# Kernel tuning notes

Measured on AMD Instinct MI355X. Metric: run time of the kernel, lower is better.

The kernel has to match this reference:

```python
import jax, jax.numpy as jnp
import numpy as np

N_NODES = 100000
D_FEAT = 64
HIDDEN = 64
N_CLASSES = 16
N_EDGES = 1600000


def setup_inputs() -> dict:
    key = jax.random.key(0)
    ks = jax.random.split(key, 8)
    x = jax.random.normal(ks[0], (N_NODES, D_FEAT), dtype=jnp.float32)
    edge_index = jax.random.randint(ks[1], (2, N_EDGES), 0, N_NODES, dtype=jnp.int64)
    s1 = 1.0 / np.sqrt(D_FEAT)
    s2 = 1.0 / np.sqrt(HIDDEN)
    W1 = jax.random.uniform(ks[2], (D_FEAT, HIDDEN), jnp.float32, -s1, s1)
    b1 = jnp.zeros((HIDDEN,), jnp.float32)
    W2 = jax.random.uniform(ks[3], (HIDDEN, HIDDEN), jnp.float32, -s2, s2)
    b2 = jnp.zeros((HIDDEN,), jnp.float32)
    Wfc = jax.random.uniform(ks[4], (HIDDEN, N_CLASSES), jnp.float32, -s2, s2)
    bfc = jax.random.uniform(ks[5], (N_CLASSES,), jnp.float32, -s2, s2)
    return {"x": x, "edge_index": edge_index, "W1": W1, "b1": b1,
            "W2": W2, "b2": b2, "Wfc": Wfc, "bfc": bfc}


def reference(x, edge_index, W1, b1, W2, b2, Wfc, bfc):
    N = x.shape[0]
    loops = jnp.arange(N, dtype=edge_index.dtype)
    # GCNConv adds self-loops by default
    src = jnp.concatenate([edge_index[0], loops])  # message source j
    dst = jnp.concatenate([edge_index[1], loops])  # aggregation target i
    # symmetric normalization: D^{-1/2} (A + I) D^{-1/2}, degree counted on targets
    deg = jax.ops.segment_sum(jnp.ones_like(dst, dtype=x.dtype), dst, num_segments=N)
    dinv = jnp.where(deg > 0, jax.lax.rsqrt(deg), 0.0)
    norm = dinv[src] * dinv[dst]  # [E+N]

    def gcn_conv(h, W, b):
        h = h @ W                              # [N, out] dense transform first (PyG order)
        msg = h[src] * norm[:, None]            # gather + edge scaling, [E+N, out]
        return jax.ops.segment_sum(msg, dst, num_segments=N) + b

    h = jax.nn.relu(gcn_conv(x, W1, b1))
    # dropout is identity in eval mode
    h = jax.nn.relu(gcn_conv(h, W2, b2))
    return jax.nn.softmax(h @ Wfc + bfc, axis=1)
```

## Files before the change

### kernel.cpp

```cpp
#include <hip/hip_runtime.h>
#include <hip/hip_fp16.h>
#include <math.h>

#define NNODES 100000
#define BSHIFT 7
#define BSIZE 128
#define NBUCK ((NNODES + BSIZE - 1) >> BSHIFT)
#define SCAT_BLOCKS 128

__global__ __launch_bounds__(256) void k_bhist(const int* __restrict__ dst, int* __restrict__ bcnt,
                                               int* __restrict__ lhout, int E, int chunk) {
    __shared__ int h[NBUCK];
    int t = threadIdx.x;
    for (int k = t; k < NBUCK; k += 256) h[k] = 0;
    __syncthreads();
    int c0 = blockIdx.x * chunk, c1 = min(E, c0 + chunk);
    for (int i = c0 + t; i < c1; i += 256)
        atomicAdd(&h[dst[i] >> BSHIFT], 1);
    __syncthreads();
    int* lh = lhout + blockIdx.x * NBUCK;
    for (int k = t; k < NBUCK; k += 256) {
        int c = h[k];
        lh[k] = c;
        if (c) atomicAdd(&bcnt[k], c);
    }
}

__global__ __launch_bounds__(1024) void k_bscan(const int* __restrict__ bcnt, int* __restrict__ bptr,
                                                int* __restrict__ bcur, int* __restrict__ rowptr,
                                                int N, int E) {
    __shared__ int s[1024];
    int t = threadIdx.x;
    int v = (t < NBUCK) ? bcnt[t] : 0;
    s[t] = v;
    __syncthreads();
    #pragma unroll
    for (int off = 1; off < 1024; off <<= 1) {
        int u = (t >= off) ? s[t - off] : 0;
        __syncthreads();
        s[t] += u;
        __syncthreads();
    }
    if (t < NBUCK) {
        int ex = s[t] - v;
        bptr[t] = ex;
        bcur[t] = ex;
    }
    if (t == 0) {
        bptr[NBUCK] = E;
        rowptr[N] = E;
    }
}

__global__ __launch_bounds__(256) void k_ms_scatter(const int* __restrict__ src, const int* __restrict__ dst,
                                                    int* __restrict__ bcur, const int* __restrict__ lhout,
                                                    int* __restrict__ staging, int E, int chunk) {
    __shared__ int lcur[NBUCK];
    int t = threadIdx.x;
    const int* lh = lhout + blockIdx.x * NBUCK;
    for (int k = t; k < NBUCK; k += 256) {
        int c = lh[k];
        lcur[k] = c ? atomicAdd(&bcur[k], c) : 0;
    }
    __syncthreads();
    int c0 = blockIdx.x * chunk, c1 = min(E, c0 + chunk);
    for (int i = c0 + t; i < c1; i += 256) {
        int d = dst[i];
        int pos = atomicAdd(&lcur[d >> BSHIFT], 1);
        staging[pos] = (src[i] << BSHIFT) | (d & (BSIZE - 1));
    }
}

__global__ __launch_bounds__(256) void k_bucket_csr(const int* __restrict__ staging, const int* __restrict__ bptr,
                                                    int* __restrict__ rowptr, int* __restrict__ ssort,
                                                    float* __restrict__ dinv, int N) {
    __shared__ int lcnt[BSIZE], lpre[BSIZE];
    int b = blockIdx.x, t = threadIdx.x;
    int node0 = b << BSHIFT;
    int bbase = bptr[b], bend = bptr[b + 1];
    if (t < BSIZE) lcnt[t] = 0;
    __syncthreads();
    for (int e = bbase + t; e < bend; e += 256)
        atomicAdd(&lcnt[staging[e] & (BSIZE - 1)], 1);
    __syncthreads();
    if (t < BSIZE) lpre[t] = lcnt[t];
    __syncthreads();
    #pragma unroll
    for (int off = 1; off < BSIZE; off <<= 1) {
        int u = 0;
        if (t < BSIZE && t >= off) u = lpre[t - off];
        __syncthreads();
        if (t < BSIZE) lpre[t] += u;
        __syncthreads();
    }
    if (t < BSIZE) {
        int node = node0 + t;
        if (node < N) {
            rowptr[node] = bbase + lpre[t] - lcnt[t];
            dinv[node] = rsqrtf((float)(lcnt[t] + 1));
        }
        lpre[t] -= lcnt[t];
    }
    __syncthreads();
    for (int e = bbase + t; e < bend; e += 256) {
        int p = staging[e];
        int pos = atomicAdd(&lpre[p & (BSIZE - 1)], 1);
        ssort[bbase + pos] = p >> BSHIFT;
    }
}

__global__ __launch_bounds__(128) void k_transform2(const float* __restrict__ X, const float* __restrict__ W,
                                                    const float* __restrict__ dinv, __half* __restrict__ Gh, int N) {
    __shared__ float Xs[128 * 65];
    __shared__ float Ws[64 * 64];
    int t = threadIdx.x;
    int node0 = blockIdx.x << 7;
    {
        const float4* W4 = (const float4*)W;
        float4* Ws4 = (float4*)Ws;
        #pragma unroll
        for (int j = 0; j < 8; j++) Ws4[j * 128 + t] = W4[j * 128 + t];
    }
    {
        const float4* X4 = (const float4*)X;
        int lim4 = N << 4;
        #pragma unroll
        for (int ii = 0; ii < 16; ii++) {
            int f = ii * 128 + t;
            int row = f >> 4, cq = f & 15;
            int gi = (node0 << 4) + f;
            float4 v = make_float4(0.f, 0.f, 0.f, 0.f);
            if (gi < lim4) v = X4[gi];
            *(float4*)&Xs[row * 65 + cq * 4] = v;
        }
    }
    __syncthreads();
    float acc[64];
    #pragma unroll
    for (int c = 0; c < 64; c++) acc[c] = 0.f;
    int xbase = t * 65;
    for (int k = 0; k < 64; k++) {
        float xk = Xs[xbase + k];
        const float4* wr = (const float4*)&Ws[k * 64];
        #pragma unroll
        for (int cb = 0; cb < 16; cb++) {
            float4 w4 = wr[cb];
            acc[cb * 4 + 0] = fmaf(xk, w4.x, acc[cb * 4 + 0]);
            acc[cb * 4 + 1] = fmaf(xk, w4.y, acc[cb * 4 + 1]);
            acc[cb * 4 + 2] = fmaf(xk, w4.z, acc[cb * 4 + 2]);
            acc[cb * 4 + 3] = fmaf(xk, w4.w, acc[cb * 4 + 3]);
        }
    }
    int node = node0 + t;
    if (node < N) {
        float di = dinv[node];
        float4* g4 = (float4*)(Gh + (size_t)node * 64);
        #pragma unroll
        for (int cb = 0; cb < 8; cb++) {
            float4 pack;
            __half2* hp = (__half2*)&pack;
            #pragma unroll
            for (int q = 0; q < 4; q++)
                hp[q] = __floats2half2_rn(acc[cb * 8 + 2 * q] * di, acc[cb * 8 + 2 * q + 1] * di);
            g4[cb] = pack;
        }
    }
}

__global__ __launch_bounds__(256) void k_agg(const __half* __restrict__ G, const int* __restrict__ rowptr,
                                             const int* __restrict__ ssort, const float* __restrict__ dinv,
                                             const float* __restrict__ bias, float* __restrict__ O, int N) {
    int lane = threadIdx.x & 63;
    int wid = threadIdx.x >> 6;
    int sub = lane >> 3;
    int l = lane & 7;
    int i = blockIdx.x * 4 + wid;
    if (i >= N) return;
    int beg = rowptr[i], end = rowptr[i + 1];
    float a[8] = {0.f, 0.f, 0.f, 0.f, 0.f, 0.f, 0.f, 0.f};
    int e = beg + sub;
    for (; e + 8 < end; e += 16) {
        int s0 = ssort[e];
        int s1 = ssort[e + 8];
        float4 g0 = *(const float4*)(G + (size_t)s0 * 64 + 8 * l);
        float4 g1 = *(const float4*)(G + (size_t)s1 * 64 + 8 * l);
        const __half2* h0 = (const __half2*)&g0;
        const __half2* h1 = (const __half2*)&g1;
        #pragma unroll
        for (int q = 0; q < 4; q++) {
            float2 f0 = __half22float2(h0[q]);
            float2 f1 = __half22float2(h1[q]);
            a[2 * q]     += f0.x + f1.x;
            a[2 * q + 1] += f0.y + f1.y;
        }
    }
    if (e < end) {
        int s0 = ssort[e];
        float4 g0 = *(const float4*)(G + (size_t)s0 * 64 + 8 * l);
        const __half2* h0 = (const __half2*)&g0;
        #pragma unroll
        for (int q = 0; q < 4; q++) {
            float2 f0 = __half22float2(h0[q]);
            a[2 * q]     += f0.x;
            a[2 * q + 1] += f0.y;
        }
    }
    #pragma unroll
    for (int mask = 8; mask <= 32; mask <<= 1) {
        #pragma unroll
        for (int q = 0; q < 8; q++) a[q] += __shfl_xor(a[q], mask);
    }
    if (sub == 0) {
        float4 gs = *(const float4*)(G + (size_t)i * 64 + 8 * l);
        const __half2* hs = (const __half2*)&gs;
        #pragma unroll
        for (int q = 0; q < 4; q++) {
            float2 fs = __half22float2(hs[q]);
            a[2 * q]     += fs.x;
            a[2 * q + 1] += fs.y;
        }
        float di = dinv[i];
        float4 b0 = *(const float4*)(bias + 8 * l);
        float4 b1 = *(const float4*)(bias + 8 * l + 4);
        float4 o0, o1;
        o0.x = fmaxf(fmaf(di, a[0], b0.x), 0.f);
        o0.y = fmaxf(fmaf(di, a[1], b0.y), 0.f);
        o0.z = fmaxf(fmaf(di, a[2], b0.z), 0.f);
        o0.w = fmaxf(fmaf(di, a[3], b0.w), 0.f);
        o1.x = fmaxf(fmaf(di, a[4], b1.x), 0.f);
        o1.y = fmaxf(fmaf(di, a[5], b1.y), 0.f);
        o1.z = fmaxf(fmaf(di, a[6], b1.z), 0.f);
        o1.w = fmaxf(fmaf(di, a[7], b1.w), 0.f);
        *(float4*)(O + (size_t)i * 64 + 8 * l) = o0;
        *(float4*)(O + (size_t)i * 64 + 8 * l + 4) = o1;
    }
}

__global__ __launch_bounds__(256) void k_fc_softmax(const float* __restrict__ H, const float* __restrict__ Wfc,
                                                    const float* __restrict__ bfc, float* __restrict__ O, int N) {
    __shared__ float wf[64 * 16];
    __shared__ float bf[16];
    int t = threadIdx.x;
    for (int k = t; k < 1024; k += 256) wf[k] = Wfc[k];
    if (t < 16) bf[t] = bfc[t];
    __syncthreads();
    int gid = blockIdx.x * 256 + t;
    int node = gid >> 4;
    int c = gid & 15;
    if (node >= N) return;
    const float4* hv = (const float4*)(H + (size_t)node * 64);
    float acc = bf[c];
    #pragma unroll
    for (int kk = 0; kk < 16; kk++) {
        float4 h4 = hv[kk];
        acc = fmaf(h4.x, wf[(4 * kk + 0) * 16 + c], acc);
        acc = fmaf(h4.y, wf[(4 * kk + 1) * 16 + c], acc);
        acc = fmaf(h4.z, wf[(4 * kk + 2) * 16 + c], acc);
        acc = fmaf(h4.w, wf[(4 * kk + 3) * 16 + c], acc);
    }
    float m = acc;
    #pragma unroll
    for (int mask = 1; mask < 16; mask <<= 1) m = fmaxf(m, __shfl_xor(m, mask));
    float ex = expf(acc - m);
    float s = ex;
    #pragma unroll
    for (int mask = 1; mask < 16; mask <<= 1) s += __shfl_xor(s, mask);
    O[(size_t)node * 16 + c] = ex / s;
}

extern "C" void kernel_launch(void* const* d_in, const int* in_sizes, int n_in,
                              void* d_out, int out_size, void* d_ws, size_t ws_size,
                              hipStream_t stream) {
    const float* x   = (const float*)d_in[0];
    const int*   ei  = (const int*)d_in[1];
    const float* W1  = (const float*)d_in[2];
    const float* b1  = (const float*)d_in[3];
    const float* W2  = (const float*)d_in[4];
    const float* b2  = (const float*)d_in[5];
    const float* Wfc = (const float*)d_in[6];
    const float* bfc = (const float*)d_in[7];
    float* out = (float*)d_out;
    const int N = NNODES;
    const int E = in_sizes[1] / 2;

    char* ws = (char*)d_ws;
    size_t off = 0;
    auto take = [&](size_t bytes) {
        char* p = ws + off;
        off = (off + bytes + 255) & ~(size_t)255;
        return p;
    };
    float*  bufA    = (float*)take((size_t)N * 64 * 4);
    float*  bufB    = (float*)take((size_t)N * 64 * 4);
    __half* Gh      = (__half*)take((size_t)N * 64 * 2);
    int*    ssort   = (int*)take((size_t)E * 4);
    int*    rowptr  = (int*)take((size_t)(N + 1) * 4);
    float*  dinv    = (float*)take((size_t)N * 4);
    int*    bcnt    = (int*)take((size_t)(NBUCK + 1) * 4);
    int*    bptr    = (int*)take((size_t)(NBUCK + 1) * 4);
    int*    bcur    = (int*)take((size_t)NBUCK * 4);
    int*    lhout   = (int*)take((size_t)SCAT_BLOCKS * NBUCK * 4);
    int*    staging = (int*)bufA;

    const int* e_src = ei;
    const int* e_dst = ei + E;

    hipMemsetAsync(bcnt, 0, (size_t)NBUCK * 4, stream);
    int chunk = (E + SCAT_BLOCKS - 1) / SCAT_BLOCKS;
    k_bhist<<<SCAT_BLOCKS, 256, 0, stream>>>(e_dst, bcnt, lhout, E, chunk);
    k_bscan<<<1, 1024, 0, stream>>>(bcnt, bptr, bcur, rowptr, N, E);
    k_ms_scatter<<<SCAT_BLOCKS, 256, 0, stream>>>(e_src, e_dst, bcur, lhout, staging, E, chunk);
    k_bucket_csr<<<NBUCK, 256, 0, stream>>>(staging, bptr, rowptr, ssort, dinv, N);

    int tb = (N + 127) / 128;
    k_transform2<<<tb, 128, 0, stream>>>(x, W1, dinv, Gh, N);
    k_agg<<<(N + 3) / 4, 256, 0, stream>>>(Gh, rowptr, ssort, dinv, b1, bufB, N);
    k_transform2<<<tb, 128, 0, stream>>>(bufB, W2, dinv, Gh, N);
    k_agg<<<(N + 3) / 4, 256, 0, stream>>>(Gh, rowptr, ssort, dinv, b2, bufB, N);
    k_fc_softmax<<<(N * 16 + 255) / 256, 256, 0, stream>>>(bufB, Wfc, bfc, out, N);
}
```

Before: 253.5 us.

## Fuse edge bucketing into one scatter pass using fixed-capacity bucket slots

Replaces the histogram, global scan and scatter kernels with a single scatter kernel. It stages each chunk's edges in shared memory, builds a local histogram, and reserves space in per-bucket fixed-capacity regions via global atomics. Rows are then described by separate begin/end arrays instead of a dense prefix-sum rowptr. This removes a full extra pass over the destination array, a memset and two launches. In exchange it assumes no bucket exceeds its fixed capacity and that each chunk fits the shared buffer, and it uses more workspace.

```diff
diff --git a/kernel.cpp b/kernel.cpp
--- a/kernel.cpp
+++ b/kernel.cpp
@@ -6,78 +6,57 @@
 #define BSHIFT 7
 #define BSIZE 128
 #define NBUCK ((NNODES + BSIZE - 1) >> BSHIFT)
-#define SCAT_BLOCKS 128
-
-__global__ __launch_bounds__(256) void k_bhist(const int* __restrict__ dst, int* __restrict__ bcnt,
-                                               int* __restrict__ lhout, int E, int chunk) {
-    __shared__ int h[NBUCK];
-    int t = threadIdx.x;
-    for (int k = t; k < NBUCK; k += 256) h[k] = 0;
-    __syncthreads();
-    int c0 = blockIdx.x * chunk, c1 = min(E, c0 + chunk);
-    for (int i = c0 + t; i < c1; i += 256)
-        atomicAdd(&h[dst[i] >> BSHIFT], 1);
-    __syncthreads();
-    int* lh = lhout + blockIdx.x * NBUCK;
-    for (int k = t; k < NBUCK; k += 256) {
-        int c = h[k];
-        lh[k] = c;
-        if (c) atomicAdd(&bcnt[k], c);
-    }
-}
-
-__global__ __launch_bounds__(1024) void k_bscan(const int* __restrict__ bcnt, int* __restrict__ bptr,
-                                                int* __restrict__ bcur, int* __restrict__ rowptr,
-                                                int N, int E) {
-    __shared__ int s[1024];
-    int t = threadIdx.x;
-    int v = (t < NBUCK) ? bcnt[t] : 0;
-    s[t] = v;
-    __syncthreads();
-    #pragma unroll
-    for (int off = 1; off < 1024; off <<= 1) {
-        int u = (t >= off) ? s[t - off] : 0;
-        __syncthreads();
-        s[t] += u;
-        __syncthreads();
-    }
-    if (t < NBUCK) {
-        int ex = s[t] - v;
-        bptr[t] = ex;
-        bcur[t] = ex;
-    }
-    if (t == 0) {
-        bptr[NBUCK] = E;
-        rowptr[N] = E;
-    }
-}
-
-__global__ __launch_bounds__(256) void k_ms_scatter(const int* __restrict__ src, const int* __restrict__ dst,
-                                                    int* __restrict__ bcur, const int* __restrict__ lhout,
-                                                    int* __restrict__ staging, int E, int chunk) {
+#define SCAT_BLOCKS 512
+#define CHUNKCAP 3328
+#define CAPSHIFT 12
+#define BCAP (1 << CAPSHIFT)
+
+__global__ __launch_bounds__(1024) void k_init(int* __restrict__ bcur) {
+    int k = blockIdx.x * 1024 + threadIdx.x;
+    if (k < NBUCK) bcur[k] = k << CAPSHIFT;
+}
+
+__global__ __launch_bounds__(256) void k_scatter_fused(const int* __restrict__ src, const int* __restrict__ dst,
+                                                       int* __restrict__ bcur, int* __restrict__ staging,
+                                                       int E, int chunk) {
+    __shared__ int epack[CHUNKCAP];
+    __shared__ unsigned short ebuck[CHUNKCAP];
+    __shared__ int hist[NBUCK];
     __shared__ int lcur[NBUCK];
     int t = threadIdx.x;
-    const int* lh = lhout + blockIdx.x * NBUCK;
+    for (int k = t; k < NBUCK; k += 256) hist[k] = 0;
+    __syncthreads();
+    int c0 = blockIdx.x * chunk;
+    int c1 = min(E, c0 + chunk);
+    int n = c1 - c0;
+    for (int j = t; j < n; j += 256) {
+        int d = dst[c0 + j];
+        int s = src[c0 + j];
+        int b = d >> BSHIFT;
+        epack[j] = (s << BSHIFT) | (d & (BSIZE - 1));
+        ebuck[j] = (unsigned short)b;
+        atomicAdd(&hist[b], 1);
+    }
+    __syncthreads();
     for (int k = t; k < NBUCK; k += 256) {
-        int c = lh[k];
+        int c = hist[k];
         lcur[k] = c ? atomicAdd(&bcur[k], c) : 0;
     }
     __syncthreads();
-    int c0 = blockIdx.x * chunk, c1 = min(E, c0 + chunk);
-    for (int i = c0 + t; i < c1; i += 256) {
-        int d = dst[i];
-        int pos = atomicAdd(&lcur[d >> BSHIFT], 1);
-        staging[pos] = (src[i] << BSHIFT) | (d & (BSIZE - 1));
-    }
-}
-
-__global__ __launch_bounds__(256) void k_bucket_csr(const int* __restrict__ staging, const int* __restrict__ bptr,
-                                                    int* __restrict__ rowptr, int* __restrict__ ssort,
-                                                    float* __restrict__ dinv, int N) {
+    for (int j = t; j < n; j += 256) {
+        int pos = atomicAdd(&lcur[ebuck[j]], 1);
+        staging[pos] = epack[j];
+    }
+}
+
+__global__ __launch_bounds__(256) void k_bucket_csr(const int* __restrict__ staging, const int* __restrict__ bcur,
+                                                    int* __restrict__ rowptr, int* __restrict__ rowend,
+                                                    int* __restrict__ ssort, float* __restrict__ dinv, int N) {
     __shared__ int lcnt[BSIZE], lpre[BSIZE];
     int b = blockIdx.x, t = threadIdx.x;
     int node0 = b << BSHIFT;
-    int bbase = bptr[b], bend = bptr[b + 1];
+    int bbase = b << CAPSHIFT;
+    int bend = bcur[b];
     if (t < BSIZE) lcnt[t] = 0;
     __syncthreads();
     for (int e = bbase + t; e < bend; e += 256)
@@ -96,7 +75,9 @@
     if (t < BSIZE) {
         int node = node0 + t;
         if (node < N) {
-            rowptr[node] = bbase + lpre[t] - lcnt[t];
+            int beg = bbase + lpre[t] - lcnt[t];
+            rowptr[node] = beg;
+            rowend[node] = beg + lcnt[t];
             dinv[node] = rsqrtf((float)(lcnt[t] + 1));
         }
         lpre[t] -= lcnt[t];
@@ -168,15 +149,16 @@
 }
 
 __global__ __launch_bounds__(256) void k_agg(const __half* __restrict__ G, const int* __restrict__ rowptr,
-                                             const int* __restrict__ ssort, const float* __restrict__ dinv,
-                                             const float* __restrict__ bias, float* __restrict__ O, int N) {
+                                             const int* __restrict__ rowend, const int* __restrict__ ssort,
+                                             const float* __restrict__ dinv, const float* __restrict__ bias,
+                                             float* __restrict__ O, int N) {
     int lane = threadIdx.x & 63;
     int wid = threadIdx.x >> 6;
     int sub = lane >> 3;
     int l = lane & 7;
     int i = blockIdx.x * 4 + wid;
     if (i >= N) return;
-    int beg = rowptr[i], end = rowptr[i + 1];
+    int beg = rowptr[i], end = rowend[i];
     float a[8] = {0.f, 0.f, 0.f, 0.f, 0.f, 0.f, 0.f, 0.f};
     int e = beg + sub;
     for (; e + 8 < end; e += 16) {
@@ -290,32 +272,27 @@
         off = (off + bytes + 255) & ~(size_t)255;
         return p;
     };
-    float*  bufA    = (float*)take((size_t)N * 64 * 4);
+    int*    staging = (int*)take((size_t)NBUCK * BCAP * 4);
+    int*    ssort   = (int*)take((size_t)NBUCK * BCAP * 4);
     float*  bufB    = (float*)take((size_t)N * 64 * 4);
     __half* Gh      = (__half*)take((size_t)N * 64 * 2);
-    int*    ssort   = (int*)take((size_t)E * 4);
-    int*    rowptr  = (int*)take((size_t)(N + 1) * 4);
+    int*    rowptr  = (int*)take((size_t)N * 4);
+    int*    rowend  = (int*)take((size_t)N * 4);
     float*  dinv    = (float*)take((size_t)N * 4);
-    int*    bcnt    = (int*)take((size_t)(NBUCK + 1) * 4);
-    int*    bptr    = (int*)take((size_t)(NBUCK + 1) * 4);
     int*    bcur    = (int*)take((size_t)NBUCK * 4);
-    int*    lhout   = (int*)take((size_t)SCAT_BLOCKS * NBUCK * 4);
-    int*    staging = (int*)bufA;
 
     const int* e_src = ei;
     const int* e_dst = ei + E;
 
-    hipMemsetAsync(bcnt, 0, (size_t)NBUCK * 4, stream);
     int chunk = (E + SCAT_BLOCKS - 1) / SCAT_BLOCKS;
-    k_bhist<<<SCAT_BLOCKS, 256, 0, stream>>>(e_dst, bcnt, lhout, E, chunk);
-    k_bscan<<<1, 1024, 0, stream>>>(bcnt, bptr, bcur, rowptr, N, E);
-    k_ms_scatter<<<SCAT_BLOCKS, 256, 0, stream>>>(e_src, e_dst, bcur, lhout, staging, E, chunk);
-    k_bucket_csr<<<NBUCK, 256, 0, stream>>>(staging, bptr, rowptr, ssort, dinv, N);
+    k_init<<<1, 1024, 0, stream>>>(bcur);
+    k_scatter_fused<<<SCAT_BLOCKS, 256, 0, stream>>>(e_src, e_dst, bcur, staging, E, chunk);
+    k_bucket_csr<<<NBUCK, 256, 0, stream>>>(staging, bcur, rowptr, rowend, ssort, dinv, N);
 
     int tb = (N + 127) / 128;
     k_transform2<<<tb, 128, 0, stream>>>(x, W1, dinv, Gh, N);
-    k_agg<<<(N + 3) / 4, 256, 0, stream>>>(Gh, rowptr, ssort, dinv, b1, bufB, N);
+    k_agg<<<(N + 3) / 4, 256, 0, stream>>>(Gh, rowptr, rowend, ssort, dinv, b1, bufB, N);
     k_transform2<<<tb, 128, 0, stream>>>(bufB, W2, dinv, Gh, N);
-    k_agg<<<(N + 3) / 4, 256, 0, stream>>>(Gh, rowptr, ssort, dinv, b2, bufB, N);
+    k_agg<<<(N + 3) / 4, 256, 0, stream>>>(Gh, rowptr, rowend, ssort, dinv, b2, bufB, N);
     k_fc_softmax<<<(N * 16 + 255) / 256, 256, 0, stream>>>(bufB, Wfc, bfc, out, N);
 }
```

Result: faster. 224.5 us (-11.5%).
